# Optimization experiments

Measured on AMD Instinct MI355X. Metric: run time of the kernel, lower is better.

## Reference

```python
import jax, jax.numpy as jnp
import numpy as np

B, S, D = 32, 1, 4096
H, HKV, HD = 32, 8, 128
G = H // HKV            # GQA groups = 4
MAXLEN = 2048
START = 2047            # decode position; cache holds 2047 past tokens


def setup_inputs() -> dict:
    key = jax.random.key(0)
    ks = jax.random.split(key, 8)
    w_scale = 0.02
    # RoPE angles for position START (module works only for seq_len==1)
    inv_freq = 1.0 / (10000.0 ** (np.arange(0, HD, 2, dtype=np.float32) / HD))
    ang = jnp.asarray(START * inv_freq, dtype=jnp.float32)  # (HD/2,)
    return {
        "x": jax.random.normal(ks[0], (B, S, D), jnp.float32),
        "cache_k": jax.random.normal(ks[1], (B, HKV, MAXLEN, HD), jnp.float32),
        "cache_v": jax.random.normal(ks[2], (B, HKV, MAXLEN, HD), jnp.float32),
        "wq": jax.random.normal(ks[3], (D, H * HD), jnp.float32) * w_scale,
        "wk": jax.random.normal(ks[4], (D, HKV * HD), jnp.float32) * w_scale,
        "wv": jax.random.normal(ks[5], (D, HKV * HD), jnp.float32) * w_scale,
        "wo": jax.random.normal(ks[6], (H * HD, D), jnp.float32) * w_scale,
        "freqs_cos": jnp.cos(ang),
        "freqs_sin": jnp.sin(ang),
        "start_pos": START,
    }


def _rope(x, cos, sin):
    # x: (B, h, S, HD); complex multiply on interleaved (even=real, odd=imag) pairs
    xr, xi = x[..., 0::2], x[..., 1::2]
    out_r = xr * cos - xi * sin
    out_i = xr * sin + xi * cos
    return jnp.stack([out_r, out_i], axis=-1).reshape(x.shape)


def reference(x, cache_k, cache_v, wq, wk, wv, wo, freqs_cos, freqs_sin, start_pos):
    b, s, _ = x.shape
    # projections -> (B, heads, S, HD)
    q = (x @ wq).reshape(b, s, H, HD).transpose(0, 2, 1, 3)
    k = (x @ wk).reshape(b, s, HKV, HD).transpose(0, 2, 1, 3)
    v = (x @ wv).reshape(b, s, HKV, HD).transpose(0, 2, 1, 3)
    # RoPE on q and k
    q = _rope(q, freqs_cos, freqs_sin)
    k = _rope(k, freqs_cos, freqs_sin)
    # KV-cache append at start_pos
    ck = jax.lax.dynamic_update_slice(cache_k, k, (0, 0, start_pos, 0))
    cv = jax.lax.dynamic_update_slice(cache_v, v, (0, 0, start_pos, 0))
    L = start_pos + s
    keys = ck[:, :, :L]   # (B, HKV, L, HD)
    vals = cv[:, :, :L]
    # GQA: group query heads over kv heads (avoids materializing repeat_kv;
    # identical math to expand+reshape in the original)
    qg = q.reshape(b, HKV, G, s, HD)
    scale = 1.0 / np.sqrt(HD).astype(np.float32)
    scores = jnp.einsum('bkgsd,bkld->bkgsl', qg, keys) * scale
    probs = jax.nn.softmax(scores.astype(jnp.float32), axis=-1).astype(q.dtype)
    out = jnp.einsum('bkgsl,bkld->bkgsd', probs, vals)
    out = out.reshape(b, H, s, HD).transpose(0, 2, 1, 3).reshape(b, s, H * HD)
    return out @ wo
```

## Files before the change

### kernel.cpp

```cpp
#include <hip/hip_runtime.h>
#include <cmath>

#define Bb 32
#define Dm 4096
#define Hh 32
#define HKVh 8
#define HD 128
#define Gq 4
#define MAXLEN 2048
#define NQ 4096
#define NKV 1024
#define NTOT 6144
#define KSPLIT 8
#define KCH 512
#define LSPLIT 4
#define SCALE 0.08838834764831845f

__device__ __forceinline__ float4 fma4(float s, float4 w, float4 a) {
    a.x = fmaf(s, w.x, a.x); a.y = fmaf(s, w.y, a.y);
    a.z = fmaf(s, w.z, a.z); a.w = fmaf(s, w.w, a.w);
    return a;
}

__global__ __launch_bounds__(256) void k_qkv(const float* __restrict__ x,
    const float* __restrict__ wq, const float* __restrict__ wk,
    const float* __restrict__ wv, float* __restrict__ part)
{
    __shared__ float xs[Bb][KCH];
    const int ct = blockIdx.x;
    const int ks = blockIdx.y;
    const int c0 = ct * 64;
    const int k0 = ks * KCH;
    const float* Wp; int ldw; int cw;
    if (c0 < NQ)          { Wp = wq; ldw = NQ;  cw = c0; }
    else if (c0 < NQ+NKV) { Wp = wk; ldw = NKV; cw = c0 - NQ; }
    else                  { Wp = wv; ldw = NKV; cw = c0 - NQ - NKV; }

    const int t = threadIdx.x;
    for (int i = t; i < Bb * (KCH/4); i += 256) {
        int b = i >> 7;
        int kk = (i & 127) << 2;
        float4 v4 = *(const float4*)(x + (size_t)b*Dm + k0 + kk);
        xs[b][kk+0] = v4.x; xs[b][kk+1] = v4.y; xs[b][kk+2] = v4.z; xs[b][kk+3] = v4.w;
    }
    __syncthreads();

    const int cg = t & 15;
    const int bg = t >> 4;
    const int b0 = bg * 2;
    const float* wp = Wp + (size_t)k0 * ldw + cw + cg*4;
    float4 a0 = make_float4(0.f,0.f,0.f,0.f), a1 = make_float4(0.f,0.f,0.f,0.f);
#pragma unroll 2
    for (int k = 0; k < KCH; k += 4) {
        float4 w0 = *(const float4*)(wp);
        float4 w1 = *(const float4*)(wp + ldw);
        float4 w2 = *(const float4*)(wp + 2*ldw);
        float4 w3 = *(const float4*)(wp + 3*ldw);
        wp += 4*ldw;
        float4 xa = *(const float4*)(&xs[b0][k]);
        float4 xb = *(const float4*)(&xs[b0+1][k]);
        a0 = fma4(xa.x, w0, a0); a1 = fma4(xb.x, w0, a1);
        a0 = fma4(xa.y, w1, a0); a1 = fma4(xb.y, w1, a1);
        a0 = fma4(xa.z, w2, a0); a1 = fma4(xb.z, w2, a1);
        a0 = fma4(xa.w, w3, a0); a1 = fma4(xb.w, w3, a1);
    }
    size_t base = ((size_t)ks * Bb + b0) * NTOT + c0 + cg*4;
    *(float4*)(part + base) = a0;
    *(float4*)(part + base + NTOT) = a1;
}

__global__ __launch_bounds__(256) void k_rope_scatter(const float* __restrict__ part,
    const float* __restrict__ cos_, const float* __restrict__ sin_,
    const int* __restrict__ start_pos, float* __restrict__ qbuf,
    float* __restrict__ cache_k, float* __restrict__ cache_v)
{
    int idx = blockIdx.x*256 + threadIdx.x;
    int b  = idx / (NTOT/2);
    int cp = idx % (NTOT/2);
    int c = cp*2;
    float xr = 0.f, xi = 0.f;
#pragma unroll
    for (int s = 0; s < KSPLIT; ++s) {
        const float2 p = *(const float2*)(part + ((size_t)s*Bb + b)*NTOT + c);
        xr += p.x; xi += p.y;
    }
    const int sp = start_pos[0];
    if (c < NQ) {
        int h = c / HD, dd = c % HD; int fi = dd >> 1;
        float co = cos_[fi], si = sin_[fi];
        float2 o = make_float2(xr*co - xi*si, xr*si + xi*co);
        *(float2*)(qbuf + ((size_t)b*Hh + h)*HD + dd) = o;
    } else if (c < NQ+NKV) {
        int cc = c - NQ; int h = cc / HD, dd = cc % HD; int fi = dd >> 1;
        float co = cos_[fi], si = sin_[fi];
        float2 o = make_float2(xr*co - xi*si, xr*si + xi*co);
        *(float2*)(cache_k + (((size_t)b*HKVh + h)*MAXLEN + sp)*HD + dd) = o;
    } else {
        int cc = c - NQ - NKV; int h = cc / HD, dd = cc % HD;
        *(float2*)(cache_v + (((size_t)b*HKVh + h)*MAXLEN + sp)*HD + dd) = make_float2(xr, xi);
    }
}

__global__ __launch_bounds__(512) void k_attn(const float* __restrict__ qbuf,
    const float* __restrict__ cache_k, const float* __restrict__ cache_v,
    const int* __restrict__ start_pos, float* __restrict__ pout)
{
    __shared__ float sm[8][Gq];
    __shared__ float sl[8][Gq];
    __shared__ float sacc[8][Gq][HD];

    const int bk = blockIdx.x;
    const int b  = bk >> 3;
    const int kv = bk & 7;
    const int sp = blockIdx.y;
    const int L  = start_pos[0] + 1;
    const int per = (L + LSPLIT - 1) / LSPLIT;
    const int p0 = sp * per;
    const int p1 = min(L, p0 + per);

    const int t = threadIdx.x;
    const int wave = t >> 6;
    const int lane = t & 63;
    const int half = lane >> 5;
    const int dl   = lane & 31;

    float4 q4[Gq];
#pragma unroll
    for (int g = 0; g < Gq; ++g) {
        float4 qq = *(const float4*)(qbuf + ((size_t)b*Hh + kv*Gq + g)*HD + dl*4);
        qq.x *= SCALE; qq.y *= SCALE; qq.z *= SCALE; qq.w *= SCALE;
        q4[g] = qq;
    }

    const float* kbase = cache_k + ((size_t)b*HKVh + kv)*MAXLEN*HD;
    const float* vbase = cache_v + ((size_t)b*HKVh + kv)*MAXLEN*HD;

    const int nw  = (per + 7) >> 3;
    const int wp0 = p0 + wave * nw;
    const int wp1 = min(p1, wp0 + nw);

    float  m[Gq], l[Gq];
    float4 acc[Gq];
#pragma unroll
    for (int g = 0; g < Gq; ++g) {
        m[g] = -1e30f; l[g] = 0.f;
        acc[g] = make_float4(0.f, 0.f, 0.f, 0.f);
    }

    for (int pp = wp0; pp < wp1; pp += 4) {
        const int pa = pp + half;
        const int pb = pp + 2 + half;
        const bool va = pa < wp1;
        const bool vb = pb < wp1;
        const int pca = va ? pa : wp0;
        const int pcb = vb ? pb : wp0;
        const float4 kA = *(const float4*)(kbase + (size_t)pca*HD + dl*4);
        const float4 kB = *(const float4*)(kbase + (size_t)pcb*HD + dl*4);
        const float4 vA = *(const float4*)(vbase + (size_t)pca*HD + dl*4);
        const float4 vB = *(const float4*)(vbase + (size_t)pcb*HD + dl*4);

        float sA[Gq], sB[Gq];
#pragma unroll
        for (int g = 0; g < Gq; ++g) {
            sA[g] = q4[g].x*kA.x + q4[g].y*kA.y + q4[g].z*kA.z + q4[g].w*kA.w;
            sB[g] = q4[g].x*kB.x + q4[g].y*kB.y + q4[g].z*kB.z + q4[g].w*kB.w;
        }
#pragma unroll
        for (int off = 16; off; off >>= 1) {
#pragma unroll
            for (int g = 0; g < Gq; ++g) {
                sA[g] += __shfl_xor(sA[g], off);
                sB[g] += __shfl_xor(sB[g], off);
            }
        }
        if (!va) { sA[0] = -INFINITY; sA[1] = -INFINITY; sA[2] = -INFINITY; sA[3] = -INFINITY; }
        if (!vb) { sB[0] = -INFINITY; sB[1] = -INFINITY; sB[2] = -INFINITY; sB[3] = -INFINITY; }

#pragma unroll
        for (int g = 0; g < Gq; ++g) {
            float mn = fmaxf(m[g], sA[g]);
            float al = __expf(m[g] - mn);
            float e  = __expf(sA[g] - mn);
            m[g] = mn;
            l[g] = l[g]*al + e;
            acc[g].x = fmaf(e, vA.x, acc[g].x*al);
            acc[g].y = fmaf(e, vA.y, acc[g].y*al);
            acc[g].z = fmaf(e, vA.z, acc[g].z*al);
            acc[g].w = fmaf(e, vA.w, acc[g].w*al);
        }
#pragma unroll
        for (int g = 0; g < Gq; ++g) {
            float mn = fmaxf(m[g], sB[g]);
            float al = __expf(m[g] - mn);
            float e  = __expf(sB[g] - mn);
            m[g] = mn;
            l[g] = l[g]*al + e;
            acc[g].x = fmaf(e, vB.x, acc[g].x*al);
            acc[g].y = fmaf(e, vB.y, acc[g].y*al);
            acc[g].z = fmaf(e, vB.z, acc[g].z*al);
            acc[g].w = fmaf(e, vB.w, acc[g].w*al);
        }
    }

#pragma unroll
    for (int g = 0; g < Gq; ++g) {
        float mo = __shfl_xor(m[g], 32);
        float lo = __shfl_xor(l[g], 32);
        float ax = __shfl_xor(acc[g].x, 32);
        float ay = __shfl_xor(acc[g].y, 32);
        float az = __shfl_xor(acc[g].z, 32);
        float aw = __shfl_xor(acc[g].w, 32);
        float mn = fmaxf(m[g], mo);
        float a0 = __expf(m[g] - mn);
        float a1 = __expf(mo - mn);
        m[g] = mn;
        l[g] = l[g]*a0 + lo*a1;
        acc[g].x = acc[g].x*a0 + ax*a1;
        acc[g].y = acc[g].y*a0 + ay*a1;
        acc[g].z = acc[g].z*a0 + az*a1;
        acc[g].w = acc[g].w*a0 + aw*a1;
    }

    if (half == 0) {
#pragma unroll
        for (int g = 0; g < Gq; ++g) {
            *(float4*)(&sacc[wave][g][dl*4]) = acc[g];
            if (dl == 0) { sm[wave][g] = m[g]; sl[wave][g] = l[g]; }
        }
    }
    __syncthreads();

    {
        const int g = t >> 7, d = t & 127;
        float M = -1e30f;
#pragma unroll
        for (int w = 0; w < 8; ++w) M = fmaxf(M, sm[w][g]);
        float num = 0.f, den = 0.f;
#pragma unroll
        for (int w = 0; w < 8; ++w) {
            float wt = __expf(sm[w][g] - M);
            num = fmaf(wt, sacc[w][g][d], num);
            den = fmaf(wt, sl[w][g], den);
        }
        float* po = pout + (size_t)(bk * LSPLIT + sp) * (Gq*HD + 2*Gq);
        po[g*HD + d] = num;
        if (d == 0) { po[Gq*HD + g] = M; po[Gq*HD + Gq + g] = den; }
    }
}

__global__ __launch_bounds__(256) void k_comb(const float* __restrict__ pout,
    float* __restrict__ attn)
{
    int idx = blockIdx.x*256 + threadIdx.x;
    int d = idx & 127;
    int h = (idx >> 7) & 31;
    int b = idx >> 12;
    int kv = h >> 2, g = h & 3;
    int bk = b*8 + kv;
    const float* base = pout + (size_t)bk * LSPLIT * (Gq*HD + 2*Gq);
    float m = -INFINITY;
#pragma unroll
    for (int s = 0; s < LSPLIT; ++s) m = fmaxf(m, base[s*520 + 512 + g]);
    float num = 0.f, den = 0.f;
#pragma unroll
    for (int s = 0; s < LSPLIT; ++s) {
        float ms = base[s*520 + 512 + g];
        float ls = base[s*520 + 516 + g];
        float w = (ms == -INFINITY) ? 0.f : __expf(ms - m);
        num = fmaf(w, base[s*520 + g*HD + d], num);
        den = fmaf(w, ls, den);
    }
    attn[idx] = num / den;
}

__global__ __launch_bounds__(256) void k_proj(const float* __restrict__ inp,
    const float* __restrict__ W, float* __restrict__ part)
{
    __shared__ float xs[Bb][KCH];
    const int ct = blockIdx.x;
    const int ks = blockIdx.y;
    const int c0 = ct * 64;
    const int k0 = ks * KCH;

    const int t = threadIdx.x;
    for (int i = t; i < Bb * (KCH/4); i += 256) {
        int b = i >> 7;
        int kk = (i & 127) << 2;
        float4 v4 = *(const float4*)(inp + (size_t)b*NQ + k0 + kk);
        xs[b][kk+0] = v4.x; xs[b][kk+1] = v4.y; xs[b][kk+2] = v4.z; xs[b][kk+3] = v4.w;
    }
    __syncthreads();

    const int cg = t & 15;
    const int bg = t >> 4;
    const int b0 = bg * 2;
    const float* wp = W + (size_t)k0 * NQ + c0 + cg*4;
    float4 a0 = make_float4(0.f,0.f,0.f,0.f), a1 = make_float4(0.f,0.f,0.f,0.f);
#pragma unroll 2
    for (int k = 0; k < KCH; k += 4) {
        float4 w0 = *(const float4*)(wp);
        float4 w1 = *(const float4*)(wp + NQ);
        float4 w2 = *(const float4*)(wp + 2*NQ);
        float4 w3 = *(const float4*)(wp + 3*NQ);
        wp += 4*NQ;
        float4 xa = *(const float4*)(&xs[b0][k]);
        float4 xb = *(const float4*)(&xs[b0+1][k]);
        a0 = fma4(xa.x, w0, a0); a1 = fma4(xb.x, w0, a1);
        a0 = fma4(xa.y, w1, a0); a1 = fma4(xb.y, w1, a1);
        a0 = fma4(xa.z, w2, a0); a1 = fma4(xb.z, w2, a1);
        a0 = fma4(xa.w, w3, a0); a1 = fma4(xb.w, w3, a1);
    }
    size_t base = ((size_t)ks * Bb + b0) * NQ + c0 + cg*4;
    *(float4*)(part + base) = a0;
    *(float4*)(part + base + NQ) = a1;
}

__global__ __launch_bounds__(256) void k_red(const float* __restrict__ part,
    float* __restrict__ out)
{
    int idx = blockIdx.x*256 + threadIdx.x;
    float s = 0.f;
#pragma unroll
    for (int k = 0; k < KSPLIT; ++k) s += part[(size_t)k*Bb*NQ + idx];
    out[idx] = s;
}

extern "C" void kernel_launch(void* const* d_in, const int* in_sizes, int n_in,
                              void* d_out, int out_size, void* d_ws, size_t ws_size,
                              hipStream_t stream)
{
    const float* x  = (const float*)d_in[0];
    float* cache_k  = (float*)d_in[1];
    float* cache_v  = (float*)d_in[2];
    const float* wq = (const float*)d_in[3];
    const float* wk = (const float*)d_in[4];
    const float* wv = (const float*)d_in[5];
    const float* wo = (const float*)d_in[6];
    const float* fc = (const float*)d_in[7];
    const float* fs = (const float*)d_in[8];
    const int* sp   = (const int*)d_in[9];
    float* out      = (float*)d_out;

    float* ws = (float*)d_ws;
    float* qkv_part = ws;
    float* qbuf     = qkv_part + 1572864;
    float* attn_prt = qbuf + 131072;
    float* attn_out = attn_prt + 532480;
    float* proj_prt = attn_out + 131072;

    k_qkv<<<dim3(96, 8), 256, 0, stream>>>(x, wq, wk, wv, qkv_part);
    k_rope_scatter<<<dim3(384), 256, 0, stream>>>(qkv_part, fc, fs, sp, qbuf, cache_k, cache_v);
    k_attn<<<dim3(256, LSPLIT), 512, 0, stream>>>(qbuf, cache_k, cache_v, sp, attn_prt);
    k_comb<<<dim3(512), 256, 0, stream>>>(attn_prt, attn_out);
    k_proj<<<dim3(64, 8), 256, 0, stream>>>(attn_out, wo, proj_prt);
    k_red<<<dim3(512), 256, 0, stream>>>(proj_prt, out);
}
```

Measured before the change: 726.6 us.

## Use 16-lane row groups with DPP reductions and exp2 in decode attention

```diff
diff --git a/kernel.cpp b/kernel.cpp
--- a/kernel.cpp
+++ b/kernel.cpp
@@ -14,12 +14,31 @@
 #define KSPLIT 8
 #define KCH 512
 #define LSPLIT 4
-#define SCALE 0.08838834764831845f
+#define SC2 0.12753102f
 
 __device__ __forceinline__ float4 fma4(float s, float4 w, float4 a) {
     a.x = fmaf(s, w.x, a.x); a.y = fmaf(s, w.y, a.y);
     a.z = fmaf(s, w.z, a.z); a.w = fmaf(s, w.w, a.w);
     return a;
+}
+
+__device__ __forceinline__ float fast_exp2(float x) {
+#if __has_builtin(__builtin_amdgcn_exp2f)
+    return __builtin_amdgcn_exp2f(x);
+#else
+    return exp2f(x);
+#endif
+}
+
+#define DPP_ADD(x, ctrl) \
+    ((x) + __int_as_float(__builtin_amdgcn_update_dpp(0, __float_as_int(x), (ctrl), 0xf, 0xf, true)))
+
+__device__ __forceinline__ float red16(float x) {
+    x = DPP_ADD(x, 0xB1);
+    x = DPP_ADD(x, 0x4E);
+    x = DPP_ADD(x, 0x141);
+    x = DPP_ADD(x, 0x140);
+    return x;
 }
 
 __global__ __launch_bounds__(256) void k_qkv(const float* __restrict__ x,
@@ -121,15 +140,18 @@
     const int t = threadIdx.x;
     const int wave = t >> 6;
     const int lane = t & 63;
-    const int half = lane >> 5;
-    const int dl   = lane & 31;
-
-    float4 q4[Gq];
+    const int sg   = lane >> 4;
+    const int dl   = lane & 15;
+
+    float4 qa[Gq], qb[Gq];
 #pragma unroll
     for (int g = 0; g < Gq; ++g) {
-        float4 qq = *(const float4*)(qbuf + ((size_t)b*Hh + kv*Gq + g)*HD + dl*4);
-        qq.x *= SCALE; qq.y *= SCALE; qq.z *= SCALE; qq.w *= SCALE;
-        q4[g] = qq;
+        const float* qp = qbuf + ((size_t)b*Hh + kv*Gq + g)*HD + dl*4;
+        float4 x0 = *(const float4*)(qp);
+        float4 x1 = *(const float4*)(qp + 64);
+        x0.x *= SC2; x0.y *= SC2; x0.z *= SC2; x0.w *= SC2;
+        x1.x *= SC2; x1.y *= SC2; x1.z *= SC2; x1.w *= SC2;
+        qa[g] = x0; qb[g] = x1;
     }
 
     const float* kbase = cache_k + ((size_t)b*HKVh + kv)*MAXLEN*HD;
@@ -140,92 +162,123 @@
     const int wp1 = min(p1, wp0 + nw);
 
     float  m[Gq], l[Gq];
-    float4 acc[Gq];
+    float4 acc0[Gq], acc1[Gq];
 #pragma unroll
     for (int g = 0; g < Gq; ++g) {
         m[g] = -1e30f; l[g] = 0.f;
-        acc[g] = make_float4(0.f, 0.f, 0.f, 0.f);
-    }
-
-    for (int pp = wp0; pp < wp1; pp += 4) {
-        const int pa = pp + half;
-        const int pb = pp + 2 + half;
-        const bool va = pa < wp1;
-        const bool vb = pb < wp1;
-        const int pca = va ? pa : wp0;
-        const int pcb = vb ? pb : wp0;
-        const float4 kA = *(const float4*)(kbase + (size_t)pca*HD + dl*4);
-        const float4 kB = *(const float4*)(kbase + (size_t)pcb*HD + dl*4);
-        const float4 vA = *(const float4*)(vbase + (size_t)pca*HD + dl*4);
-        const float4 vB = *(const float4*)(vbase + (size_t)pcb*HD + dl*4);
+        acc0[g] = make_float4(0.f,0.f,0.f,0.f);
+        acc1[g] = make_float4(0.f,0.f,0.f,0.f);
+    }
+
+    for (int pp = wp0; pp < wp1; pp += 8) {
+        const int pA = pp + sg;
+        const int pB = pp + 4 + sg;
+        const bool vA = pA < wp1;
+        const bool vB = pB < wp1;
+        const int cA = vA ? pA : wp0;
+        const int cB = vB ? pB : wp0;
+        const float* krA = kbase + (size_t)cA*HD + dl*4;
+        const float* krB = kbase + (size_t)cB*HD + dl*4;
+        const float* vrA = vbase + (size_t)cA*HD + dl*4;
+        const float* vrB = vbase + (size_t)cB*HD + dl*4;
+        const float4 ka0 = *(const float4*)(krA);
+        const float4 ka1 = *(const float4*)(krA + 64);
+        const float4 kb0 = *(const float4*)(krB);
+        const float4 kb1 = *(const float4*)(krB + 64);
+        const float4 va0 = *(const float4*)(vrA);
+        const float4 va1 = *(const float4*)(vrA + 64);
+        const float4 vb0 = *(const float4*)(vrB);
+        const float4 vb1 = *(const float4*)(vrB + 64);
 
         float sA[Gq], sB[Gq];
 #pragma unroll
         for (int g = 0; g < Gq; ++g) {
-            sA[g] = q4[g].x*kA.x + q4[g].y*kA.y + q4[g].z*kA.z + q4[g].w*kA.w;
-            sB[g] = q4[g].x*kB.x + q4[g].y*kB.y + q4[g].z*kB.z + q4[g].w*kB.w;
-        }
-#pragma unroll
-        for (int off = 16; off; off >>= 1) {
-#pragma unroll
-            for (int g = 0; g < Gq; ++g) {
-                sA[g] += __shfl_xor(sA[g], off);
-                sB[g] += __shfl_xor(sB[g], off);
-            }
-        }
-        if (!va) { sA[0] = -INFINITY; sA[1] = -INFINITY; sA[2] = -INFINITY; sA[3] = -INFINITY; }
-        if (!vb) { sB[0] = -INFINITY; sB[1] = -INFINITY; sB[2] = -INFINITY; sB[3] = -INFINITY; }
+            float a = qa[g].x*ka0.x + qa[g].y*ka0.y + qa[g].z*ka0.z + qa[g].w*ka0.w;
+            a = fmaf(qb[g].x, ka1.x, a); a = fmaf(qb[g].y, ka1.y, a);
+            a = fmaf(qb[g].z, ka1.z, a); a = fmaf(qb[g].w, ka1.w, a);
+            sA[g] = red16(a);
+            float bq = qa[g].x*kb0.x + qa[g].y*kb0.y + qa[g].z*kb0.z + qa[g].w*kb0.w;
+            bq = fmaf(qb[g].x, kb1.x, bq); bq = fmaf(qb[g].y, kb1.y, bq);
+            bq = fmaf(qb[g].z, kb1.z, bq); bq = fmaf(qb[g].w, kb1.w, bq);
+            sB[g] = red16(bq);
+        }
+        if (!vA) { sA[0] = -INFINITY; sA[1] = -INFINITY; sA[2] = -INFINITY; sA[3] = -INFINITY; }
+        if (!vB) { sB[0] = -INFINITY; sB[1] = -INFINITY; sB[2] = -INFINITY; sB[3] = -INFINITY; }
 
 #pragma unroll
         for (int g = 0; g < Gq; ++g) {
             float mn = fmaxf(m[g], sA[g]);
-            float al = __expf(m[g] - mn);
-            float e  = __expf(sA[g] - mn);
+            float al = fast_exp2(m[g] - mn);
+            float e  = fast_exp2(sA[g] - mn);
             m[g] = mn;
-            l[g] = l[g]*al + e;
-            acc[g].x = fmaf(e, vA.x, acc[g].x*al);
-            acc[g].y = fmaf(e, vA.y, acc[g].y*al);
-            acc[g].z = fmaf(e, vA.z, acc[g].z*al);
-            acc[g].w = fmaf(e, vA.w, acc[g].w*al);
+            l[g] = fmaf(l[g], al, e);
+            acc0[g].x = fmaf(e, va0.x, acc0[g].x*al);
+            acc0[g].y = fmaf(e, va0.y, acc0[g].y*al);
+            acc0[g].z = fmaf(e, va0.z, acc0[g].z*al);
+            acc0[g].w = fmaf(e, va0.w, acc0[g].w*al);
+            acc1[g].x = fmaf(e, va1.x, acc1[g].x*al);
+            acc1[g].y = fmaf(e, va1.y, acc1[g].y*al);
+            acc1[g].z = fmaf(e, va1.z, acc1[g].z*al);
+            acc1[g].w = fmaf(e, va1.w, acc1[g].w*al);
         }
 #pragma unroll
         for (int g = 0; g < Gq; ++g) {
             float mn = fmaxf(m[g], sB[g]);
-            float al = __expf(m[g] - mn);
-            float e  = __expf(sB[g] - mn);
+            float al = fast_exp2(m[g] - mn);
+            float e  = fast_exp2(sB[g] - mn);
             m[g] = mn;
-            l[g] = l[g]*al + e;
-            acc[g].x = fmaf(e, vB.x, acc[g].x*al);
-            acc[g].y = fmaf(e, vB.y, acc[g].y*al);
-            acc[g].z = fmaf(e, vB.z, acc[g].z*al);
-            acc[g].w = fmaf(e, vB.w, acc[g].w*al);
+            l[g] = fmaf(l[g], al, e);
+            acc0[g].x = fmaf(e, vb0.x, acc0[g].x*al);
+            acc0[g].y = fmaf(e, vb0.y, acc0[g].y*al);
+            acc0[g].z = fmaf(e, vb0.z, acc0[g].z*al);
+            acc0[g].w = fmaf(e, vb0.w, acc0[g].w*al);
+            acc1[g].x = fmaf(e, vb1.x, acc1[g].x*al);
+            acc1[g].y = fmaf(e, vb1.y, acc1[g].y*al);
+            acc1[g].z = fmaf(e, vb1.z, acc1[g].z*al);
+            acc1[g].w = fmaf(e, vb1.w, acc1[g].w*al);
         }
     }
 
 #pragma unroll
     for (int g = 0; g < Gq; ++g) {
-        float mo = __shfl_xor(m[g], 32);
-        float lo = __shfl_xor(l[g], 32);
-        float ax = __shfl_xor(acc[g].x, 32);
-        float ay = __shfl_xor(acc[g].y, 32);
-        float az = __shfl_xor(acc[g].z, 32);
-        float aw = __shfl_xor(acc[g].w, 32);
-        float mn = fmaxf(m[g], mo);
-        float a0 = __expf(m[g] - mn);
-        float a1 = __expf(mo - mn);
-        m[g] = mn;
-        l[g] = l[g]*a0 + lo*a1;
-        acc[g].x = acc[g].x*a0 + ax*a1;
-        acc[g].y = acc[g].y*a0 + ay*a1;
-        acc[g].z = acc[g].z*a0 + az*a1;
-        acc[g].w = acc[g].w*a0 + aw*a1;
-    }
-
-    if (half == 0) {
+#pragma unroll
+        for (int st = 0; st < 2; ++st) {
+            const int off = st ? 32 : 16;
+            float mo = __shfl_xor(m[g], off);
+            float lo = __shfl_xor(l[g], off);
+            float o0x = __shfl_xor(acc0[g].x, off);
+            float o0y = __shfl_xor(acc0[g].y, off);
+            float o0z = __shfl_xor(acc0[g].z, off);
+            float o0w = __shfl_xor(acc0[g].w, off);
+            float o1x = __shfl_xor(acc1[g].x, off);
+            float o1y = __shfl_xor(acc1[g].y, off);
+            float o1z = __shfl_xor(acc1[g].z, off);
+            float o1w = __shfl_xor(acc1[g].w, off);
+            float mn = fmaxf(m[g], mo);
+            float w0 = fast_exp2(m[g] - mn);
+            float w1 = fast_exp2(mo - mn);
+            m[g] = mn;
+            l[g] = l[g]*w0 + lo*w1;
+            acc0[g].x = acc0[g].x*w0 + o0x*w1;
+            acc0[g].y = acc0[g].y*w0 + o0y*w1;
+            acc0[g].z = acc0[g].z*w0 + o0z*w1;
+            acc0[g].w = acc0[g].w*w0 + o0w*w1;
+            acc1[g].x = acc1[g].x*w0 + o1x*w1;
+            acc1[g].y = acc1[g].y*w0 + o1y*w1;
+            acc1[g].z = acc1[g].z*w0 + o1z*w1;
+            acc1[g].w = acc1[g].w*w0 + o1w*w1;
+        }
+    }
+
+    if (lane < 16) {
 #pragma unroll
         for (int g = 0; g < Gq; ++g) {
-            *(float4*)(&sacc[wave][g][dl*4]) = acc[g];
-            if (dl == 0) { sm[wave][g] = m[g]; sl[wave][g] = l[g]; }
+            *(float4*)(&sacc[wave][g][dl*4])      = acc0[g];
+            *(float4*)(&sacc[wave][g][64 + dl*4]) = acc1[g];
+        }
+        if (lane == 0) {
+#pragma unroll
+            for (int g = 0; g < Gq; ++g) { sm[wave][g] = m[g]; sl[wave][g] = l[g]; }
         }
     }
     __syncthreads();
@@ -238,7 +291,7 @@
         float num = 0.f, den = 0.f;
 #pragma unroll
         for (int w = 0; w < 8; ++w) {
-            float wt = __expf(sm[w][g] - M);
+            float wt = fast_exp2(sm[w][g] - M);
             num = fmaf(wt, sacc[w][g][d], num);
             den = fmaf(wt, sl[w][g], den);
         }
@@ -266,7 +319,7 @@
     for (int s = 0; s < LSPLIT; ++s) {
         float ms = base[s*520 + 512 + g];
         float ls = base[s*520 + 516 + g];
-        float w = (ms == -INFINITY) ? 0.f : __expf(ms - m);
+        float w = (ms == -INFINITY) ? 0.f : fast_exp2(ms - m);
         num = fmaf(w, base[s*520 + g*HD + d], num);
         den = fmaf(w, ls, den);
     }
```

Measured after the change: 720.2 us. About the same (-0.9%).
